# Kernel optimization log

Hardware: AMD Instinct MI355X
Metric: run time of the kernel (lower is better)

## Reference

```python
import jax, jax.numpy as jnp
import numpy as np

EPS = 1e-5

def _mlp(x, w1, b1, w2, b2):
    # torch: Linear -> ReLU -> Linear (weights stored as (in, out))
    return jax.nn.relu(x @ w1 + b1) @ w2 + b2

def _ln(x, g, b):
    mu = x.mean(-1, keepdims=True)
    var = ((x - mu) ** 2).mean(-1, keepdims=True)
    return (x - mu) * jax.lax.rsqrt(var + EPS) * g + b

def setup_inputs():
    key = jax.random.key(0)
    B, N, d, d_out, M, K = 8, 8192, 256, 512, 2048, 16
    ks = jax.random.split(key, 16)
    def nrm(k, shape, s=0.05):
        return jax.random.normal(k, shape, jnp.float32) * s
    return dict(
        pos=jax.random.normal(ks[0], (B, N, 3), jnp.float32),
        feat=jax.random.normal(ks[1], (B, N, d), jnp.float32),
        fps_idx=jax.random.randint(ks[2], (B, M), 0, N, jnp.int32),
        knn_idx=jax.random.randint(ks[3], (B, M, K), 0, N, jnp.int32),
        cs1=16, cs2=64,
        mlp1_w1=nrm(ks[4], (2, 4, d), 0.3), mlp1_b1=jnp.zeros((2, d)),
        mlp1_w2=nrm(ks[5], (2, d, d)), mlp1_b2=jnp.zeros((2, d)),
        mlp2_w1=nrm(ks[6], (2, 6, d), 0.3), mlp2_b1=jnp.zeros((2, d)),
        mlp2_w2=nrm(ks[7], (2, d, d)), mlp2_b2=jnp.zeros((2, d)),
        wq=nrm(ks[8], (2, d, d)), wk=nrm(ks[9], (2, d, d)),
        wv=nrm(ks[10], (2, d, d)), wo=nrm(ks[11], (2, d, d)), bo=jnp.zeros((2, d)),
        ln_g=jnp.ones((2, d)), ln_b=jnp.zeros((2, d)),
        td_w=nrm(ks[12], (d, d_out)), td_b=jnp.zeros((d_out,)),
        bn_g=jnp.ones((d_out,)), bn_b=jnp.zeros((d_out,)),
        bn_mean=jnp.zeros((d_out,)), bn_var=jnp.ones((d_out,)),
    )

def reference(pos, feat, fps_idx, knn_idx, cs1, cs2,
              mlp1_w1, mlp1_b1, mlp1_w2, mlp1_b2,
              mlp2_w1, mlp2_b1, mlp2_w2, mlp2_b2,
              wq, wk, wv, wo, bo, ln_g, ln_b,
              td_w, td_b, bn_g, bn_b, bn_mean, bn_var):
    def block(f_in, cs, i):
        # DLPTBlock with equal-size contiguous clusters of size cs.
        # Note: original forward returns ln1(h_pos + dlsa_out); the ff branch is dead code.
        B, N, d = f_in.shape
        nc = N // cs
        pc = pos.reshape(B, nc, cs, 3)
        fc = f_in.reshape(B, nc, cs, d)
        cog = pc.mean(axis=2, keepdims=True)         # per-cluster center of gravity
        lp = pc - cog                                # local coords
        nrm = jnp.linalg.norm(lp, axis=-1, keepdims=True)
        h_pos = fc + _mlp(jnp.concatenate([lp, nrm], -1),
                          mlp1_w1[i], mlp1_b1[i], mlp1_w2[i], mlp1_b2[i])
        avg = jnp.broadcast_to(lp.mean(axis=2, keepdims=True), lp.shape)
        h_geo = fc + _mlp(jnp.concatenate([avg, lp], -1),
                          mlp2_w1[i], mlp2_b1[i], mlp2_w2[i], mlp2_b2[i])
        q = (h_geo @ wq[i]) / jnp.sqrt(jnp.float32(d))
        k = h_geo @ wk[i]
        v = h_pos @ wv[i]
        a = jax.nn.softmax(jnp.einsum('bcqd,bckd->bcqk', q, k), axis=-1)
        out = jnp.einsum('bcqk,bckd->bcqd', a, v) @ wo[i] + bo[i]
        return _ln(h_pos + out, ln_g[i], ln_b[i]).reshape(B, N, d)

    f = block(feat, cs1, 0)
    f = block(f, cs2, 1)
    # TransitionDown: linear -> BN (eval, running stats) -> relu -> knn max-pool
    f = f @ td_w + td_b
    f = jax.nn.relu((f - bn_mean) * jax.lax.rsqrt(bn_var + EPS) * bn_g + bn_b)
    pos_ds = jnp.take_along_axis(pos, fps_idx[..., None], axis=1)   # (B, M, 3)
    B = f.shape[0]
    f_knn = f[jnp.arange(B)[:, None, None], knn_idx]                # (B, M, K, d_out)
    feat_ds = f_knn.max(axis=2)
    return (pos_ds, feat_ds)
```

## Files before the change

### kernel.cpp

```cpp
#include <hip/hip_runtime.h>
#include <stdint.h>
#include <stddef.h>

typedef __attribute__((ext_vector_type(8))) short bf16x8;
typedef __attribute__((ext_vector_type(4))) float f32x4;
typedef __attribute__((ext_vector_type(8))) unsigned short u16x8;
typedef __attribute__((ext_vector_type(4))) unsigned short u16x4;
typedef __attribute__((ext_vector_type(2))) unsigned short u16x2;

#define DEVINL __device__ __forceinline__

DEVINL unsigned short f2b(float x){
  union { float f; unsigned int u; } v; v.f = x;
  return (unsigned short)((v.u + 0x7FFFu + ((v.u >> 16) & 1u)) >> 16);
}
DEVINL float b2f(unsigned short h){
  union { float f; unsigned int u; } v; v.u = ((unsigned int)h) << 16;
  return v.f;
}

DEVINL void gl_lds16(void* g, void* lds){
  __builtin_amdgcn_global_load_lds(
      (__attribute__((address_space(1))) void*)g,
      (__attribute__((address_space(3))) void*)lds, 16, 0, 0);
}

__global__ __launch_bounds__(256) void prep_k(
    const float* __restrict__ m1w2, const float* __restrict__ m2w2,
    const float* __restrict__ wqp,  const float* __restrict__ wkp,
    const float* __restrict__ wvp,  const float* __restrict__ wop,
    const float* __restrict__ tdw,  const float* __restrict__ tdb,
    const float* __restrict__ bng,  const float* __restrict__ bnb,
    const float* __restrict__ bnm,  const float* __restrict__ bnv,
    unsigned short* __restrict__ wT, float* __restrict__ bns, float* __restrict__ bnt)
{
  int idx = blockIdx.x * 256 + threadIdx.x;
  if (idx < 786432){
    int mat = idx >> 17;
    int e   = idx & 131071;
    int i   = e >> 16;
    int eb  = e & 65535;
    int n = eb >> 8, kx = eb & 255;
    const float* src; float sc = 1.0f;
    if      (mat == 0) src = m1w2;
    else if (mat == 1) src = m2w2;
    else if (mat == 2){ src = wqp; sc = 0.0625f; }
    else if (mat == 3) src = wkp;
    else if (mat == 4) src = wvp;
    else               src = wop;
    wT[idx] = f2b(src[i*65536 + kx*256 + n] * sc);
  } else if (idx < 917504){
    int e = idx - 786432;
    int n = e >> 8, kx = e & 255;
    wT[786432 + e] = f2b(tdw[kx*512 + n]);
  } else if (idx < 918016){
    int c = idx - 917504;
    float s = bng[c] * rsqrtf(bnv[c] + 1e-5f);
    bns[c] = s;
    bnt[c] = (tdb[c] - bnm[c]) * s + bnb[c];
  }
}

__global__ __launch_bounds__(256) void gemm_k(
    const unsigned short* __restrict__ A,
    const unsigned short* __restrict__ Wt,
    unsigned short* __restrict__ out,
    const float* __restrict__ bias,
    const unsigned short* __restrict__ addend,
    const float* __restrict__ bn_s,
    const float* __restrict__ bn_t,
    int ldc)
{
  __shared__ __attribute__((aligned(16))) unsigned short aT[512*8];
  __shared__ __attribute__((aligned(16))) unsigned short bT[512*8];
  __shared__ __attribute__((aligned(16))) unsigned short epi[128*140];

  const int tid  = threadIdx.x;
  const int lane = tid & 63;
  const int wave = tid >> 6;
  const int lrow = lane & 15, lq = lane >> 4;
  const int wr = wave >> 1, wc = wave & 1;
  const int m0 = blockIdx.x * 128;
  const int n0 = blockIdx.y * 128;

  f32x4 acc[4][4] = {};

  int aOff[4], bOff[4];
#pragma unroll
  for (int mt = 0; mt < 4; mt++){
    int row = wr*64 + mt*16 + lrow;
    aOff[mt] = row*64 + ((lq ^ ((row >> 1) & 3)) << 4);
  }
#pragma unroll
  for (int nt = 0; nt < 4; nt++){
    int row = wc*64 + nt*16 + lrow;
    bOff[nt] = row*64 + ((lq ^ ((row >> 1) & 3)) << 4);
  }

  const int s0 = tid, s1 = tid + 256;
  const int r0 = s0 >> 2, kc0 = (s0 & 3) ^ ((r0 >> 1) & 3);
  const int r1 = s1 >> 2, kc1 = (s1 & 3) ^ ((r1 >> 1) & 3);
  const unsigned short* Ab = A  + (size_t)m0 * 256;
  const unsigned short* Bb = Wt + (size_t)n0 * 256;
  char* aL = (char*)aT;
  char* bL = (char*)bT;
  const int wslot = wave * 64 * 16;

  for (int k0 = 0; k0 < 256; k0 += 32){
    __syncthreads();
    gl_lds16((void*)(Ab + r0*256 + k0 + kc0*8), aL + wslot);
    gl_lds16((void*)(Ab + r1*256 + k0 + kc1*8), aL + 4096 + wslot);
    gl_lds16((void*)(Bb + r0*256 + k0 + kc0*8), bL + wslot);
    gl_lds16((void*)(Bb + r1*256 + k0 + kc1*8), bL + 4096 + wslot);
    __syncthreads();
    bf16x8 af[4], bfr[4];
#pragma unroll
    for (int mt = 0; mt < 4; mt++) af[mt]  = *(const bf16x8*)(aL + aOff[mt]);
#pragma unroll
    for (int nt = 0; nt < 4; nt++) bfr[nt] = *(const bf16x8*)(bL + bOff[nt]);
#pragma unroll
    for (int mt = 0; mt < 4; mt++)
#pragma unroll
      for (int nt = 0; nt < 4; nt++)
        acc[mt][nt] = __builtin_amdgcn_mfma_f32_16x16x32_bf16(af[mt], bfr[nt], acc[mt][nt], 0, 0, 0);
  }

  __syncthreads();
#pragma unroll
  for (int mt = 0; mt < 4; mt++){
    int row = wr*64 + mt*16 + lq*4;
#pragma unroll
    for (int nt = 0; nt < 4; nt++){
      int col = wc*64 + nt*16 + lrow;
#pragma unroll
      for (int r = 0; r < 4; r++)
        epi[(row + r)*140 + col] = f2b(acc[mt][nt][r]);
    }
  }
  __syncthreads();

  const int erow = tid >> 1, h = tid & 1;
  const size_t gbase = (size_t)(m0 + erow) * (size_t)ldc + n0;
#pragma unroll
  for (int i = 0; i < 8; i++){
    int col = h*64 + i*8;
    u16x4 lo = *(const u16x4*)(&epi[erow*140 + col]);
    u16x4 hi = *(const u16x4*)(&epi[erow*140 + col + 4]);
    float y[8];
#pragma unroll
    for (int j = 0; j < 4; j++){ y[j] = b2f(lo[j]); y[4+j] = b2f(hi[j]); }
    if (addend){
      u16x8 ad = *(const u16x8*)(addend + gbase + col);
#pragma unroll
      for (int j = 0; j < 8; j++) y[j] += b2f(ad[j]);
    }
    if (bias){
#pragma unroll
      for (int j = 0; j < 8; j++) y[j] += bias[n0 + col + j];
    }
    if (bn_s){
#pragma unroll
      for (int j = 0; j < 8; j++){
        float t2 = y[j]*bn_s[n0 + col + j] + bn_t[n0 + col + j];
        y[j] = fmaxf(t2, 0.f);
      }
    }
    u16x8 o;
#pragma unroll
    for (int j = 0; j < 8; j++) o[j] = f2b(y[j]);
    *(u16x8*)(out + gbase + col) = o;
  }
}

DEVINL void wg_gemm1(const unsigned short* __restrict__ Wt,
                     const char* Als, int tid, f32x4 (&acc)[4])
{
  const int lane = tid & 63;
  const int wave = tid >> 6;
  const int lrow = lane & 15, lq = lane >> 4;
  const unsigned short* base = Wt + (size_t)(wave*16 + lrow)*256 + lq*8;

  bf16x8 bn = *(const bf16x8*)(base);
#pragma unroll
  for (int k = 0; k < 8; k++){
    bf16x8 b = bn;
    if (k < 7) bn = *(const bf16x8*)(base + (k+1)*32);
#pragma unroll
    for (int mt = 0; mt < 4; mt++){
      int row = mt*16 + lrow;
      bf16x8 af = *(const bf16x8*)(Als + row*512 + ((k*64 + lq*16) ^ ((row & 7) << 4)));
      acc[mt] = __builtin_amdgcn_mfma_f32_16x16x32_bf16(af, b, acc[mt], 0, 0, 0);
    }
  }
}

DEVINL void wg_epi_fc1(f32x4 (&acc)[4], char* Yls, const float* __restrict__ bias,
                       const unsigned int (&fcp)[4][2], int tid)
{
  const int lane = tid & 63, wave = tid >> 6;
  const int lrow = lane & 15, lq = lane >> 4;
  const int col = wave*16 + lrow;
  const float bv = bias[col];
#pragma unroll
  for (int mt = 0; mt < 4; mt++){
#pragma unroll
    for (int p = 0; p < 2; p++){
      unsigned int f = fcp[mt][p];
      int row0 = mt*16 + lq*4 + 2*p;
      int row1 = row0 + 1;
      float y0 = acc[mt][2*p]   + bv + b2f((unsigned short)f);
      float y1 = acc[mt][2*p+1] + bv + b2f((unsigned short)(f >> 16));
      *(unsigned short*)(Yls + row0*512 + ((col*2) ^ ((row0 & 7) << 4))) = f2b(y0);
      *(unsigned short*)(Yls + row1*512 + ((col*2) ^ ((row1 & 7) << 4))) = f2b(y1);
    }
  }
}

DEVINL void wg_epi_regs1(f32x4 (&acc)[4], const float* __restrict__ bias,
                         const unsigned int (&fcp)[4][2], unsigned int (&hp)[4][2],
                         int tid)
{
  const int lane = tid & 63, wave = tid >> 6;
  const int lrow = lane & 15;
  const int col = wave*16 + lrow;
  const float bv = bias[col];
#pragma unroll
  for (int mt = 0; mt < 4; mt++){
#pragma unroll
    for (int p = 0; p < 2; p++){
      unsigned int f = fcp[mt][p];
      float y0 = acc[mt][2*p]   + bv + b2f((unsigned short)f);
      float y1 = acc[mt][2*p+1] + bv + b2f((unsigned short)(f >> 16));
      hp[mt][p] = (unsigned int)f2b(y0) | ((unsigned int)f2b(y1) << 16);
    }
  }
}

DEVINL void wg_epi_plain1(f32x4 (&acc)[4], char* Yls, int tid)
{
  const int lane = tid & 63, wave = tid >> 6;
  const int lrow = lane & 15, lq = lane >> 4;
  const int col = wave*16 + lrow;
#pragma unroll
  for (int mt = 0; mt < 4; mt++){
#pragma unroll
    for (int r = 0; r < 4; r++){
      const int row = mt*16 + lq*4 + r;
      *(unsigned short*)(Yls + row*512 + ((col*2) ^ ((row & 7) << 4))) = f2b(acc[mt][r]);
    }
  }
}

DEVINL void wg_epi_vt1(f32x4 (&acc)[4], char* VT, int tid)
{
  const int lane = tid & 63, wave = tid >> 6;
  const int lrow = lane & 15, lq = lane >> 4;
  const int col = wave*16 + lrow;
#pragma unroll
  for (int mt = 0; mt < 4; mt++){
    const int row0 = mt*16 + lq*4;
    u16x4 w;
#pragma unroll
    for (int r = 0; r < 4; r++) w[r] = f2b(acc[mt][r]);
    *(u16x4*)(VT + col*128 + ((row0*2) ^ ((col & 7) << 4))) = w;
  }
}

template<int CS, bool F32IN>
__global__ __launch_bounds__(1024, 4) void block_k(
    const float* __restrict__ pos,
    const float* __restrict__ featF,
    const unsigned short* __restrict__ featB,
    const float* __restrict__ w1a, const float* __restrict__ b1a,
    const float* __restrict__ w1b, const float* __restrict__ b1b,
    const unsigned short* __restrict__ m1w2T, const float* __restrict__ m1b2,
    const unsigned short* __restrict__ m2w2T, const float* __restrict__ m2b2,
    const unsigned short* __restrict__ wqT, const unsigned short* __restrict__ wkT,
    const unsigned short* __restrict__ wvT, const unsigned short* __restrict__ woT,
    const float* __restrict__ bo, const float* __restrict__ lgam,
    const float* __restrict__ lbet,
    unsigned short* __restrict__ out)
{
  __shared__ __attribute__((aligned(16))) char smem[82240];
  char* BA = smem;
  char* BB = smem + 32768;
  char* Pm = smem + 65536;
  float (*P3)[3]    = (float(*)[3])(smem + 73728);
  float (*Cg)[3]    = (float(*)[3])(smem + 74496);
  float (*Gg)[4]    = (float(*)[4])(smem + 74560);
  float (*smx)[4]   = (float(*)[4])(smem + 75584);
  float (*ssm)[4]   = (float(*)[4])(smem + 76608);
  float (*sred)[8]  = (float(*)[8])(smem + 77632);
  float (*s2red)[8] = (float(*)[8])(smem + 79680);
  float* mub = (float*)(smem + 81728);
  float* rsb = (float*)(smem + 81984);

  const int tid  = threadIdx.x;
  const int lane = tid & 63;
  const int wave = tid >> 6;
  const int lrow = lane & 15, lq = lane >> 4;
  const int m0 = blockIdx.x * 64;

  unsigned short* gout = out + (size_t)m0 * 256;

  unsigned int fcp[4][2];
  {
    const int col = wave*16 + lrow;
    if constexpr (F32IN){
      const float* resF = featF + (size_t)m0 * 256;
#pragma unroll
      for (int mt = 0; mt < 4; mt++)
#pragma unroll
        for (int p = 0; p < 2; p++){
          int row0 = mt*16 + lq*4 + 2*p;
          unsigned int lo = f2b(resF[row0*256 + col]);
          unsigned int hi = f2b(resF[(row0+1)*256 + col]);
          fcp[mt][p] = lo | (hi << 16);
        }
    } else {
      const unsigned short* resB = featB + (size_t)m0 * 256;
#pragma unroll
      for (int mt = 0; mt < 4; mt++)
#pragma unroll
        for (int p = 0; p < 2; p++){
          int row0 = mt*16 + lq*4 + 2*p;
          unsigned int lo = resB[row0*256 + col];
          unsigned int hi = resB[(row0+1)*256 + col];
          fcp[mt][p] = lo | (hi << 16);
        }
    }
  }

  if (tid < 64){
    P3[tid][0] = pos[(size_t)(m0+tid)*3 + 0];
    P3[tid][1] = pos[(size_t)(m0+tid)*3 + 1];
    P3[tid][2] = pos[(size_t)(m0+tid)*3 + 2];
  }
  __syncthreads();

  constexpr int NCH = 64 / CS;
  if (tid < NCH*3){
    int ch = tid / 3, c = tid - ch*3;
    float s = 0.f;
    for (int r = 0; r < CS; r++) s += P3[ch*CS + r][c];
    Cg[ch][c] = s / (float)CS;
  }
  __syncthreads();
  if (tid < 64){
    int ch = (CS == 16) ? (tid >> 4) : 0;
    float x = P3[tid][0] - Cg[ch][0];
    float y = P3[tid][1] - Cg[ch][1];
    float z = P3[tid][2] - Cg[ch][2];
    Gg[tid][0] = x; Gg[tid][1] = y; Gg[tid][2] = z;
    Gg[tid][3] = sqrtf(x*x + y*y + z*z);
  }
  __syncthreads();

  {
    const int c = tid & 255;
    const int r0 = (tid >> 8) * 16;
    const float wb0 = w1b[768+c], wb1 = w1b[1024+c], wb2 = w1b[1280+c];
    const float bb  = b1b[c];
    for (int r = r0; r < r0 + 16; r++){
      float v2 = bb + Gg[r][0]*wb0 + Gg[r][1]*wb1 + Gg[r][2]*wb2;
      *(unsigned short*)(BA + r*512 + ((c*2) ^ ((r & 7) << 4))) = f2b(fmaxf(v2, 0.f));
    }
  }
  __syncthreads();
  {
    f32x4 acc[4] = {};
    wg_gemm1(m2w2T, BA, tid, acc);
    wg_epi_fc1(acc, BB, m2b2, fcp, tid);
    __syncthreads();
  }
  {
    const int c = tid & 255;
    const int r0 = (tid >> 8) * 16;
    const float wa0 = w1a[c], wa1 = w1a[256+c], wa2 = w1a[512+c], wa3 = w1a[768+c];
    const float ba  = b1a[c];
    for (int r = r0; r < r0 + 16; r++){
      float v1 = ba + Gg[r][0]*wa0 + Gg[r][1]*wa1 + Gg[r][2]*wa2 + Gg[r][3]*wa3;
      *(unsigned short*)(BA + r*512 + ((c*2) ^ ((r & 7) << 4))) = f2b(fmaxf(v1, 0.f));
    }
  }
  __syncthreads();
  unsigned int hp[4][2];
  {
    f32x4 acc[4] = {};
    wg_gemm1(m1w2T, BA, tid, acc);
    wg_epi_regs1(acc, m1b2, fcp, hp, tid);
    __syncthreads();
  }
  {
    f32x4 acc[4] = {};
    wg_gemm1(wqT, BB, tid, acc);
    wg_epi_plain1(acc, BA, tid);
    __syncthreads();
  }
  {
    f32x4 acc[4] = {};
    wg_gemm1(wkT, BB, tid, acc);
    __syncthreads();
    wg_epi_plain1(acc, BB, tid);
    __syncthreads();
  }

  if (CS == 64){
    const int tr = wave & 3, tc = wave >> 2;
    f32x4 sacc = {};
    const int qrow = tr*16 + lrow;
    const int brow = tc*16 + lrow;
    const int qsw  = (qrow & 7) << 4;
    const int bsw  = (brow & 7) << 4;
#pragma unroll
    for (int kk = 0; kk < 8; kk++){
      bf16x8 aq = *(const bf16x8*)(BA + qrow*512 + ((kk*64 + lq*16) ^ qsw));
      bf16x8 bk = *(const bf16x8*)(BB + brow*512 + ((kk*64 + lq*16) ^ bsw));
      sacc = __builtin_amdgcn_mfma_f32_16x16x32_bf16(aq, bk, sacc, 0, 0, 0);
    }
#pragma unroll
    for (int r = 0; r < 4; r++){
      float m = sacc[r];
#pragma unroll
      for (int d = 1; d < 16; d <<= 1) m = fmaxf(m, __shfl_xor(m, d));
      float e = __expf(sacc[r] - m);
      sacc[r] = e;
      float s = e;
#pragma unroll
      for (int d = 1; d < 16; d <<= 1) s += __shfl_xor(s, d);
      if (lrow == 0){
        int row = tr*16 + lq*4 + r;
        smx[row][tc] = m;
        ssm[row][tc] = s;
      }
    }
    __syncthreads();
#pragma unroll
    for (int r = 0; r < 4; r++){
      int row = tr*16 + lq*4 + r;
      float m0v = smx[row][0], m1v = smx[row][1], m2v = smx[row][2], m3v = smx[row][3];
      float M = fmaxf(fmaxf(m0v, m1v), fmaxf(m2v, m3v));
      float S = ssm[row][0]*__expf(m0v - M) + ssm[row][1]*__expf(m1v - M)
              + ssm[row][2]*__expf(m2v - M) + ssm[row][3]*__expf(m3v - M);
      float f = __expf(smx[row][tc] - M) / S;
      int col = tc*16 + lrow;
      *(unsigned short*)(Pm + row*128 + ((col*2) ^ ((row & 7) << 4))) = f2b(sacc[r]*f);
    }
    __syncthreads();
  } else {
    if (wave < 4){
      f32x4 sacc = {};
      const int qrow = wave*16 + lrow;
      const int qsw  = (qrow & 7) << 4;
#pragma unroll
      for (int kk = 0; kk < 8; kk++){
        bf16x8 aq = *(const bf16x8*)(BA + qrow*512 + ((kk*64 + lq*16) ^ qsw));
        bf16x8 bk = *(const bf16x8*)(BB + qrow*512 + ((kk*64 + lq*16) ^ qsw));
        sacc = __builtin_amdgcn_mfma_f32_16x16x32_bf16(aq, bk, sacc, 0, 0, 0);
      }
#pragma unroll
      for (int r = 0; r < 4; r++){
        float m = sacc[r];
#pragma unroll
        for (int d = 1; d < 16; d <<= 1) m = fmaxf(m, __shfl_xor(m, d));
        float e = __expf(sacc[r] - m);
        float s = e;
#pragma unroll
        for (int d = 1; d < 16; d <<= 1) s += __shfl_xor(s, d);
        int row = wave*16 + lq*4 + r;
        *(unsigned short*)(Pm + row*64 + ((lrow*2) ^ ((row & 3) << 4))) = f2b(e / s);
      }
    } else if (tid < 512){
      int t2 = tid - 256;
      int row = t2 >> 2, j = t2 & 3;
      u16x4 z = {};
      *(u16x4*)(Pm + row*64 + ((32 + j*8) ^ ((row & 3) << 4))) = z;
    }
    __syncthreads();
  }

  {
    const int col = wave*16 + lrow;
#pragma unroll
    for (int mt = 0; mt < 4; mt++)
#pragma unroll
      for (int p = 0; p < 2; p++){
        int row0 = mt*16 + lq*4 + 2*p;
        int row1 = row0 + 1;
        unsigned int d = hp[mt][p];
        *(unsigned short*)(BA + row0*512 + ((col*2) ^ ((row0 & 7) << 4))) = (unsigned short)d;
        *(unsigned short*)(BA + row1*512 + ((col*2) ^ ((row1 & 7) << 4))) = (unsigned short)(d >> 16);
      }
  }
  __syncthreads();
  {
    f32x4 acc[4] = {};
    wg_gemm1(wvT, BA, tid, acc);
    wg_epi_vt1(acc, BB, tid);
    __syncthreads();
  }

  {
    f32x4 oacc[4] = {};
    const int d = wave*16 + lrow;
    const int dsw = (d & 7) << 4;
    if (CS == 64){
#pragma unroll
      for (int kk = 0; kk < 2; kk++){
        bf16x8 bv = *(const bf16x8*)(BB + d*128 + ((kk*64 + lq*16) ^ dsw));
#pragma unroll
        for (int mt = 0; mt < 4; mt++){
          int row = mt*16 + lrow;
          bf16x8 ap = *(const bf16x8*)(Pm + row*128 + ((kk*64 + lq*16) ^ ((row & 7) << 4)));
          oacc[mt] = __builtin_amdgcn_mfma_f32_16x16x32_bf16(ap, bv, oacc[mt], 0, 0, 0);
        }
      }
    } else {
#pragma unroll
      for (int mt = 0; mt < 4; mt++){
        int row = mt*16 + lrow;
        bf16x8 ap = *(const bf16x8*)(Pm + row*64 + ((lq*16) ^ ((row & 3) << 4)));
        bf16x8 bv = *(const bf16x8*)(BB + d*128 + ((mt*32 + (lq & 1)*16) ^ dsw));
        oacc[mt] = __builtin_amdgcn_mfma_f32_16x16x32_bf16(ap, bv, oacc[mt], 0, 0, 0);
      }
    }
#pragma unroll
    for (int mt = 0; mt < 4; mt++){
#pragma unroll
      for (int r = 0; r < 4; r++){
        int row = mt*16 + lq*4 + r;
        *(unsigned short*)(BA + row*512 + ((d*2) ^ ((row & 7) << 4))) = f2b(oacc[mt][r]);
      }
    }
    __syncthreads();
  }

  {
    f32x4 yacc[4] = {};
    wg_gemm1(woT, BA, tid, yacc);
    __syncthreads();
    const int col = wave*16 + lrow;
    const float bov = bo[col];
#pragma unroll
    for (int mt = 0; mt < 4; mt++){
#pragma unroll
      for (int p = 0; p < 2; p++){
        int row0 = mt*16 + lq*4 + 2*p;
        int row1 = row0 + 1;
        unsigned int d = hp[mt][p];
        float z0 = yacc[mt][2*p]   + bov + b2f((unsigned short)d);
        float z1 = yacc[mt][2*p+1] + bov + b2f((unsigned short)(d >> 16));
        *(unsigned short*)(BA + row0*512 + ((col*2) ^ ((row0 & 7) << 4))) = f2b(z0);
        *(unsigned short*)(BA + row1*512 + ((col*2) ^ ((row1 & 7) << 4))) = f2b(z1);
      }
    }
    __syncthreads();
  }
  {
    const int row = (tid >> 3) & 63, part = tid & 7;
    const size_t gr = (size_t)row * 256;
    const int sw = (row & 7) << 4;
    if (tid < 512){
      float sm = 0.f, sq = 0.f;
#pragma unroll
      for (int i = 0; i < 4; i++){
        int col = part*32 + i*8;
        u16x8 v = *(const u16x8*)(BA + row*512 + ((col*2) ^ sw));
#pragma unroll
        for (int j = 0; j < 8; j++){
          float y = b2f(v[j]);
          sm += y; sq += y*y;
        }
      }
      sred[row][part] = sm; s2red[row][part] = sq;
    }
    __syncthreads();
    if (tid < 64){
      float s = 0.f, q2 = 0.f;
#pragma unroll
      for (int p = 0; p < 8; p++){ s += sred[tid][p]; q2 += s2red[tid][p]; }
      float mu = s * (1.0f/256.0f);
      float var = q2 * (1.0f/256.0f) - mu*mu;
      mub[tid] = mu;
      rsb[tid] = rsqrtf(var + 1e-5f);
    }
    __syncthreads();
    if (tid < 512){
      const float mu = mub[row], rs = rsb[row];
#pragma unroll
      for (int i = 0; i < 4; i++){
        int col = part*32 + i*8;
        u16x8 v = *(const u16x8*)(BA + row*512 + ((col*2) ^ sw));
        u16x8 o;
#pragma unroll
        for (int j = 0; j < 8; j++)
          o[j] = f2b((b2f(v[j]) - mu)*rs*lgam[col + j] + lbet[col + j]);
        *(u16x8*)(gout + gr + col) = o;
      }
    }
  }
}

__global__ __launch_bounds__(256) void out_k(
    const unsigned short* __restrict__ F2,
    const float* __restrict__ pos,
    const int* __restrict__ fps,
    const int* __restrict__ knn,
    float* __restrict__ outp)
{
  const int p = blockIdx.x;
  const int b = p >> 11;
  const int t = threadIdx.x;
  const int* kn = knn + (size_t)p * 16;
  const int c = t * 2;
  float m1 = -3.0e38f, m2 = -3.0e38f;
  for (int j = 0; j < 16; j++){
    int idx = kn[j];
    size_t row = ((size_t)b * 8192 + idx) * 512;
    u16x2 v = *(const u16x2*)(F2 + row + c);
    m1 = fmaxf(m1, b2f(v.x));
    m2 = fmaxf(m2, b2f(v.y));
  }
  float* of = outp + 49152 + (size_t)p * 512 + c;
  float2 o; o.x = m1; o.y = m2;
  *(float2*)of = o;
  if (t < 3){
    int fi = fps[p];
    outp[(size_t)p*3 + t] = pos[((size_t)b*8192 + fi)*3 + t];
  }
}

extern "C" void kernel_launch(void* const* d_in, const int* in_sizes, int n_in,
                              void* d_out, int out_size, void* d_ws, size_t ws_size,
                              hipStream_t stream)
{
  (void)in_sizes; (void)n_in; (void)out_size; (void)ws_size;

  const float* pos  = (const float*)d_in[0];
  const float* feat = (const float*)d_in[1];
  const int*   fps  = (const int*)d_in[2];
  const int*   knn  = (const int*)d_in[3];
  const float* m1w1 = (const float*)d_in[6];
  const float* m1b1 = (const float*)d_in[7];
  const float* m1w2 = (const float*)d_in[8];
  const float* m1b2 = (const float*)d_in[9];
  const float* m2w1 = (const float*)d_in[10];
  const float* m2b1 = (const float*)d_in[11];
  const float* m2w2 = (const float*)d_in[12];
  const float* m2b2 = (const float*)d_in[13];
  const float* wq   = (const float*)d_in[14];
  const float* wk   = (const float*)d_in[15];
  const float* wv   = (const float*)d_in[16];
  const float* wo   = (const float*)d_in[17];
  const float* bo   = (const float*)d_in[18];
  const float* lng  = (const float*)d_in[19];
  const float* lnb  = (const float*)d_in[20];
  const float* tdw  = (const float*)d_in[21];
  const float* tdb  = (const float*)d_in[22];
  const float* bng  = (const float*)d_in[23];
  const float* bnb  = (const float*)d_in[24];
  const float* bnm  = (const float*)d_in[25];
  const float* bnv  = (const float*)d_in[26];

  char* ws = (char*)d_ws;
  unsigned short* wT = (unsigned short*)ws;
  float* bns = (float*)(ws + 1835008);
  float* bnt = (float*)(ws + 1837056);
  const size_t SLOT = 33554432;
  unsigned short* A  = (unsigned short*)(ws + 2097152);
  unsigned short* Bs = (unsigned short*)(ws + 2097152 + SLOT);
  unsigned short* E  = (unsigned short*)(ws + 2097152 + 2*SLOT);

  auto wtm = [&](int mat, int i){ return wT + (size_t)mat*131072 + (size_t)i*65536; };
  unsigned short* tdT = wT + 786432;

  prep_k<<<3586, 256, 0, stream>>>(m1w2, m2w2, wq, wk, wv, wo, tdw, tdb, bng, bnb, bnm, bnv,
                                   wT, bns, bnt);

  block_k<16, true><<<1024, 1024, 0, stream>>>(
      pos, feat, nullptr,
      m1w1, m1b1, m2w1, m2b1,
      wtm(0,0), m1b2, wtm(1,0), m2b2,
      wtm(2,0), wtm(3,0), wtm(4,0), wtm(5,0),
      bo, lng, lnb, A);

  block_k<64, false><<<1024, 1024, 0, stream>>>(
      pos, nullptr, A,
      m1w1 + 1024, m1b1 + 256, m2w1 + 1536, m2b1 + 256,
      wtm(0,1), m1b2 + 256, wtm(1,1), m2b2 + 256,
      wtm(2,1), wtm(3,1), wtm(4,1), wtm(5,1),
      bo + 256, lng + 256, lnb + 256, Bs);

  gemm_k<<<dim3(512,4), 256, 0, stream>>>(Bs, tdT, E, nullptr, nullptr, bns, bnt, 512);

  out_k<<<16384, 256, 0, stream>>>(E, pos, fps, knn, (float*)d_out);
}
```

Baseline: 566.5 us.

## Split workgroup into two wave roles running independent GEMMs concurrently

The 16 waves are split into two groups of eight, each computing 64x32 output tiles, so independent GEMM pairs (the two MLP second layers, then Q and K projections) run side by side. This removes several barrier-separated sequential phases. LDS grows from about 82KB to 148KB with four ping-pong buffers, and the residual features are re-read from global memory in the epilogues instead of being held in registers. The extra LDS allows fewer resident workgroups per CU, and the output projection now runs on only half the waves.

```diff
diff --git a/kernel.cpp b/kernel.cpp
--- a/kernel.cpp
+++ b/kernel.cpp
@@ -172,97 +172,139 @@
   }
 }
 
-DEVINL void wg_gemm1(const unsigned short* __restrict__ Wt,
-                     const char* Als, int tid, f32x4 (&acc)[4])
-{
-  const int lane = tid & 63;
-  const int wave = tid >> 6;
+DEVINL void wg_gemm2(const unsigned short* __restrict__ Wt,
+                     const char* Als, int wid8, int lane, f32x4 (&acc)[4][2])
+{
   const int lrow = lane & 15, lq = lane >> 4;
-  const unsigned short* base = Wt + (size_t)(wave*16 + lrow)*256 + lq*8;
-
-  bf16x8 bn = *(const bf16x8*)(base);
+  const unsigned short* base0 = Wt + (size_t)(wid8*32 + lrow)*256 + lq*8;
+  const unsigned short* base1 = base0 + 16*256;
+
+  bf16x8 bn0 = *(const bf16x8*)(base0);
+  bf16x8 bn1 = *(const bf16x8*)(base1);
 #pragma unroll
   for (int k = 0; k < 8; k++){
-    bf16x8 b = bn;
-    if (k < 7) bn = *(const bf16x8*)(base + (k+1)*32);
+    bf16x8 b0 = bn0, b1 = bn1;
+    if (k < 7){
+      bn0 = *(const bf16x8*)(base0 + (k+1)*32);
+      bn1 = *(const bf16x8*)(base1 + (k+1)*32);
+    }
 #pragma unroll
     for (int mt = 0; mt < 4; mt++){
       int row = mt*16 + lrow;
       bf16x8 af = *(const bf16x8*)(Als + row*512 + ((k*64 + lq*16) ^ ((row & 7) << 4)));
-      acc[mt] = __builtin_amdgcn_mfma_f32_16x16x32_bf16(af, b, acc[mt], 0, 0, 0);
-    }
-  }
-}
-
-DEVINL void wg_epi_fc1(f32x4 (&acc)[4], char* Yls, const float* __restrict__ bias,
-                       const unsigned int (&fcp)[4][2], int tid)
-{
-  const int lane = tid & 63, wave = tid >> 6;
+      acc[mt][0] = __builtin_amdgcn_mfma_f32_16x16x32_bf16(af, b0, acc[mt][0], 0, 0, 0);
+      acc[mt][1] = __builtin_amdgcn_mfma_f32_16x16x32_bf16(af, b1, acc[mt][1], 0, 0, 0);
+    }
+  }
+}
+
+template<bool F32RES>
+DEVINL void wg_epi_fcg(f32x4 (&acc)[4][2], char* Yls, const float* __restrict__ bias,
+                       const float* __restrict__ resF,
+                       const unsigned short* __restrict__ resB,
+                       int wid8, int lane)
+{
   const int lrow = lane & 15, lq = lane >> 4;
-  const int col = wave*16 + lrow;
-  const float bv = bias[col];
 #pragma unroll
   for (int mt = 0; mt < 4; mt++){
 #pragma unroll
-    for (int p = 0; p < 2; p++){
-      unsigned int f = fcp[mt][p];
-      int row0 = mt*16 + lq*4 + 2*p;
-      int row1 = row0 + 1;
-      float y0 = acc[mt][2*p]   + bv + b2f((unsigned short)f);
-      float y1 = acc[mt][2*p+1] + bv + b2f((unsigned short)(f >> 16));
-      *(unsigned short*)(Yls + row0*512 + ((col*2) ^ ((row0 & 7) << 4))) = f2b(y0);
-      *(unsigned short*)(Yls + row1*512 + ((col*2) ^ ((row1 & 7) << 4))) = f2b(y1);
-    }
-  }
-}
-
-DEVINL void wg_epi_regs1(f32x4 (&acc)[4], const float* __restrict__ bias,
-                         const unsigned int (&fcp)[4][2], unsigned int (&hp)[4][2],
-                         int tid)
-{
-  const int lane = tid & 63, wave = tid >> 6;
-  const int lrow = lane & 15;
-  const int col = wave*16 + lrow;
-  const float bv = bias[col];
+    for (int nt = 0; nt < 2; nt++){
+      const int col = wid8*32 + nt*16 + lrow;
+      const float bv = bias[col];
+#pragma unroll
+      for (int r = 0; r < 4; r++){
+        const int row = mt*16 + lq*4 + r;
+        float fc = F32RES ? resF[row*256 + col] : b2f(resB[row*256 + col]);
+        float y = acc[mt][nt][r] + bv + fc;
+        *(unsigned short*)(Yls + row*512 + ((col*2) ^ ((row & 7) << 4))) = f2b(y);
+      }
+    }
+  }
+}
+
+template<bool F32RES>
+DEVINL void wg_epi_regs_fcg(f32x4 (&acc)[4][2], const float* __restrict__ bias,
+                            const float* __restrict__ resF,
+                            const unsigned short* __restrict__ resB,
+                            unsigned int (&hp)[4][2][2], int wid8, int lane)
+{
+  const int lrow = lane & 15, lq = lane >> 4;
 #pragma unroll
   for (int mt = 0; mt < 4; mt++){
 #pragma unroll
-    for (int p = 0; p < 2; p++){
-      unsigned int f = fcp[mt][p];
-      float y0 = acc[mt][2*p]   + bv + b2f((unsigned short)f);
-      float y1 = acc[mt][2*p+1] + bv + b2f((unsigned short)(f >> 16));
-      hp[mt][p] = (unsigned int)f2b(y0) | ((unsigned int)f2b(y1) << 16);
-    }
-  }
-}
-
-DEVINL void wg_epi_plain1(f32x4 (&acc)[4], char* Yls, int tid)
-{
-  const int lane = tid & 63, wave = tid >> 6;
+    for (int nt = 0; nt < 2; nt++){
+      const int col = wid8*32 + nt*16 + lrow;
+      const float bv = bias[col];
+#pragma unroll
+      for (int p = 0; p < 2; p++){
+        int row0 = mt*16 + lq*4 + 2*p;
+        float fc0 = F32RES ? resF[row0*256 + col] : b2f(resB[row0*256 + col]);
+        float fc1 = F32RES ? resF[(row0+1)*256 + col] : b2f(resB[(row0+1)*256 + col]);
+        float y0 = acc[mt][nt][2*p]   + bv + fc0;
+        float y1 = acc[mt][nt][2*p+1] + bv + fc1;
+        hp[mt][nt][p] = (unsigned int)f2b(y0) | ((unsigned int)f2b(y1) << 16);
+      }
+    }
+  }
+}
+
+DEVINL void wg_epi_plain2(f32x4 (&acc)[4][2], char* Yls, int wid8, int lane)
+{
   const int lrow = lane & 15, lq = lane >> 4;
-  const int col = wave*16 + lrow;
 #pragma unroll
   for (int mt = 0; mt < 4; mt++){
 #pragma unroll
-    for (int r = 0; r < 4; r++){
-      const int row = mt*16 + lq*4 + r;
-      *(unsigned short*)(Yls + row*512 + ((col*2) ^ ((row & 7) << 4))) = f2b(acc[mt][r]);
-    }
-  }
-}
-
-DEVINL void wg_epi_vt1(f32x4 (&acc)[4], char* VT, int tid)
-{
-  const int lane = tid & 63, wave = tid >> 6;
+    for (int nt = 0; nt < 2; nt++){
+      const int col = wid8*32 + nt*16 + lrow;
+#pragma unroll
+      for (int r = 0; r < 4; r++){
+        const int row = mt*16 + lq*4 + r;
+        *(unsigned short*)(Yls + row*512 + ((col*2) ^ ((row & 7) << 4))) = f2b(acc[mt][nt][r]);
+      }
+    }
+  }
+}
+
+DEVINL void wg_gemm_v(const unsigned short* __restrict__ Wt,
+                      const char* Als, int wm, int wn, int lane, f32x4 (&acc)[2][2])
+{
   const int lrow = lane & 15, lq = lane >> 4;
-  const int col = wave*16 + lrow;
-#pragma unroll
-  for (int mt = 0; mt < 4; mt++){
-    const int row0 = mt*16 + lq*4;
-    u16x4 w;
-#pragma unroll
-    for (int r = 0; r < 4; r++) w[r] = f2b(acc[mt][r]);
-    *(u16x4*)(VT + col*128 + ((row0*2) ^ ((col & 7) << 4))) = w;
+  const unsigned short* base0 = Wt + (size_t)(wn*32 + lrow)*256 + lq*8;
+  const unsigned short* base1 = base0 + 16*256;
+
+  bf16x8 bn0 = *(const bf16x8*)(base0);
+  bf16x8 bn1 = *(const bf16x8*)(base1);
+#pragma unroll
+  for (int k = 0; k < 8; k++){
+    bf16x8 b0 = bn0, b1 = bn1;
+    if (k < 7){
+      bn0 = *(const bf16x8*)(base0 + (k+1)*32);
+      bn1 = *(const bf16x8*)(base1 + (k+1)*32);
+    }
+#pragma unroll
+    for (int mt = 0; mt < 2; mt++){
+      int row = wm*32 + mt*16 + lrow;
+      bf16x8 af = *(const bf16x8*)(Als + row*512 + ((k*64 + lq*16) ^ ((row & 7) << 4)));
+      acc[mt][0] = __builtin_amdgcn_mfma_f32_16x16x32_bf16(af, b0, acc[mt][0], 0, 0, 0);
+      acc[mt][1] = __builtin_amdgcn_mfma_f32_16x16x32_bf16(af, b1, acc[mt][1], 0, 0, 0);
+    }
+  }
+}
+
+DEVINL void wg_epi_vt2(f32x4 (&acc)[2][2], char* VT, int wm, int wn, int lane)
+{
+  const int lrow = lane & 15, lq = lane >> 4;
+#pragma unroll
+  for (int mt = 0; mt < 2; mt++){
+#pragma unroll
+    for (int nt = 0; nt < 2; nt++){
+      const int col  = wn*32 + nt*16 + lrow;
+      const int row0 = wm*32 + mt*16 + lq*4;
+      u16x4 w;
+#pragma unroll
+      for (int r = 0; r < 4; r++) w[r] = f2b(acc[mt][nt][r]);
+      *(u16x4*)(VT + col*128 + ((row0*2) ^ ((col & 7) << 4))) = w;
+    }
   }
 }
 
@@ -281,55 +323,35 @@
     const float* __restrict__ lbet,
     unsigned short* __restrict__ out)
 {
-  __shared__ __attribute__((aligned(16))) char smem[82240];
-  char* BA = smem;
-  char* BB = smem + 32768;
-  char* Pm = smem + 65536;
-  float (*P3)[3]    = (float(*)[3])(smem + 73728);
-  float (*Cg)[3]    = (float(*)[3])(smem + 74496);
-  float (*Gg)[4]    = (float(*)[4])(smem + 74560);
-  float (*smx)[4]   = (float(*)[4])(smem + 75584);
-  float (*ssm)[4]   = (float(*)[4])(smem + 76608);
-  float (*sred)[8]  = (float(*)[8])(smem + 77632);
-  float (*s2red)[8] = (float(*)[8])(smem + 79680);
-  float* mub = (float*)(smem + 81728);
-  float* rsb = (float*)(smem + 81984);
+  __shared__ __attribute__((aligned(16))) char smem[147776];
+  char* B0 = smem;
+  char* B1 = smem + 32768;
+  char* B2 = smem + 65536;
+  char* B3 = smem + 98304;
+  char* Pm = smem + 131072;
+  float (*P3)[3]    = (float(*)[3])(smem + 139264);
+  float (*Cg)[3]    = (float(*)[3])(smem + 140032);
+  float (*Gg)[4]    = (float(*)[4])(smem + 140096);
+  float (*smx)[4]   = (float(*)[4])(smem + 141120);
+  float (*ssm)[4]   = (float(*)[4])(smem + 142144);
+  float (*sred)[8]  = (float(*)[8])(smem + 143168);
+  float (*s2red)[8] = (float(*)[8])(smem + 145216);
+  float* mub = (float*)(smem + 147264);
+  float* rsb = (float*)(smem + 147520);
 
   const int tid  = threadIdx.x;
   const int lane = tid & 63;
   const int wave = tid >> 6;
+  const int wid8 = wave & 7;
+  const int role = wave >> 3;
   const int lrow = lane & 15, lq = lane >> 4;
   const int m0 = blockIdx.x * 64;
 
   unsigned short* gout = out + (size_t)m0 * 256;
-
-  unsigned int fcp[4][2];
-  {
-    const int col = wave*16 + lrow;
-    if constexpr (F32IN){
-      const float* resF = featF + (size_t)m0 * 256;
-#pragma unroll
-      for (int mt = 0; mt < 4; mt++)
-#pragma unroll
-        for (int p = 0; p < 2; p++){
-          int row0 = mt*16 + lq*4 + 2*p;
-          unsigned int lo = f2b(resF[row0*256 + col]);
-          unsigned int hi = f2b(resF[(row0+1)*256 + col]);
-          fcp[mt][p] = lo | (hi << 16);
-        }
-    } else {
-      const unsigned short* resB = featB + (size_t)m0 * 256;
-#pragma unroll
-      for (int mt = 0; mt < 4; mt++)
-#pragma unroll
-        for (int p = 0; p < 2; p++){
-          int row0 = mt*16 + lq*4 + 2*p;
-          unsigned int lo = resB[row0*256 + col];
-          unsigned int hi = resB[(row0+1)*256 + col];
-          fcp[mt][p] = lo | (hi << 16);
-        }
-    }
-  }
+  const float* resF = nullptr;
+  const unsigned short* resB = nullptr;
+  if constexpr (F32IN) resF = featF + (size_t)m0 * 256;
+  else                 resB = featB + (size_t)m0 * 256;
 
   if (tid < 64){
     P3[tid][0] = pos[(size_t)(m0+tid)*3 + 0];
@@ -357,53 +379,68 @@
   __syncthreads();
 
   {
-    const int c = tid & 255;
-    const int r0 = (tid >> 8) * 16;
-    const float wb0 = w1b[768+c], wb1 = w1b[1024+c], wb2 = w1b[1280+c];
-    const float bb  = b1b[c];
-    for (int r = r0; r < r0 + 16; r++){
-      float v2 = bb + Gg[r][0]*wb0 + Gg[r][1]*wb1 + Gg[r][2]*wb2;
-      *(unsigned short*)(BA + r*512 + ((c*2) ^ ((r & 7) << 4))) = f2b(fmaxf(v2, 0.f));
-    }
-  }
-  __syncthreads();
+    if (tid < 512){
+      const int c = tid & 255;
+      const int r0 = (tid >> 8) * 32;
+      const float wb0 = w1b[768+c], wb1 = w1b[1024+c], wb2 = w1b[1280+c];
+      const float bb  = b1b[c];
+      for (int r = r0; r < r0 + 32; r++){
+        float v2 = bb + Gg[r][0]*wb0 + Gg[r][1]*wb1 + Gg[r][2]*wb2;
+        *(unsigned short*)(B0 + r*512 + ((c*2) ^ ((r & 7) << 4))) = f2b(fmaxf(v2, 0.f));
+      }
+    } else {
+      const int t = tid - 512;
+      const int c = t & 255;
+      const int r0 = (t >> 8) * 32;
+      const float wa0 = w1a[c], wa1 = w1a[256+c], wa2 = w1a[512+c], wa3 = w1a[768+c];
+      const float ba  = b1a[c];
+      for (int r = r0; r < r0 + 32; r++){
+        float v1 = ba + Gg[r][0]*wa0 + Gg[r][1]*wa1 + Gg[r][2]*wa2 + Gg[r][3]*wa3;
+        *(unsigned short*)(B1 + r*512 + ((c*2) ^ ((r & 7) << 4))) = f2b(fmaxf(v1, 0.f));
+      }
+    }
+  }
+  __syncthreads();
+
+  unsigned int hp[4][2][2];
   {
-    f32x4 acc[4] = {};
-    wg_gemm1(m2w2T, BA, tid, acc);
-    wg_epi_fc1(acc, BB, m2b2, fcp, tid);
-    __syncthreads();
-  }
+    if (role == 0){
+      f32x4 acc[4][2] = {};
+      wg_gemm2(m2w2T, B0, wid8, lane, acc);
+      wg_epi_fcg<F32IN>(acc, B2, m2b2, resF, resB, wid8, lane);
+    } else {
+      f32x4 acc[4][2] = {};
+      wg_gemm2(m1w2T, B1, wid8, lane, acc);
+      wg_epi_regs_fcg<F32IN>(acc, m1b2, resF, resB, hp, wid8, lane);
+    }
+  }
+  __syncthreads();
+
   {
-    const int c = tid & 255;
-    const int r0 = (tid >> 8) * 16;
-    const float wa0 = w1a[c], wa1 = w1a[256+c], wa2 = w1a[512+c], wa3 = w1a[768+c];
-    const float ba  = b1a[c];
-    for (int r = r0; r < r0 + 16; r++){
-      float v1 = ba + Gg[r][0]*wa0 + Gg[r][1]*wa1 + Gg[r][2]*wa2 + Gg[r][3]*wa3;
-      *(unsigned short*)(BA + r*512 + ((c*2) ^ ((r & 7) << 4))) = f2b(fmaxf(v1, 0.f));
-    }
-  }
-  __syncthreads();
-  unsigned int hp[4][2];
-  {
-    f32x4 acc[4] = {};
-    wg_gemm1(m1w2T, BA, tid, acc);
-    wg_epi_regs1(acc, m1b2, fcp, hp, tid);
-    __syncthreads();
-  }
-  {
-    f32x4 acc[4] = {};
-    wg_gemm1(wqT, BB, tid, acc);
-    wg_epi_plain1(acc, BA, tid);
-    __syncthreads();
-  }
-  {
-    f32x4 acc[4] = {};
-    wg_gemm1(wkT, BB, tid, acc);
-    __syncthreads();
-    wg_epi_plain1(acc, BB, tid);
-    __syncthreads();
-  }
+    if (role == 0){
+      f32x4 acc[4][2] = {};
+      wg_gemm2(wqT, B2, wid8, lane, acc);
+      wg_epi_plain2(acc, B1, wid8, lane);
+    } else {
+#pragma unroll
+      for (int mt = 0; mt < 4; mt++)
+#pragma unroll
+        for (int nt = 0; nt < 2; nt++)
+#pragma unroll
+          for (int p = 0; p < 2; p++){
+            int col = wid8*32 + nt*16 + lrow;
+            int row0 = mt*16 + lq*4 + 2*p;
+            int row1 = row0 + 1;
+            unsigned int d = hp[mt][nt][p];
+            *(unsigned short*)(B0 + row0*512 + ((col*2) ^ ((row0 & 7) << 4))) = (unsigned short)d;
+            *(unsigned short*)(B0 + row1*512 + ((col*2) ^ ((row1 & 7) << 4))) = (unsigned short)(d >> 16);
+          }
+      f32x4 acc[4][2] = {};
+      wg_gemm2(wkT, B2, wid8, lane, acc);
+      wg_epi_plain2(acc, B3, wid8, lane);
+    }
+  }
+  __syncthreads();
 
   if (CS == 64){
     const int tr = wave & 3, tc = wave >> 2;
@@ -414,8 +451,8 @@
     const int bsw  = (brow & 7) << 4;
 #pragma unroll
     for (int kk = 0; kk < 8; kk++){
-      bf16x8 aq = *(const bf16x8*)(BA + qrow*512 + ((kk*64 + lq*16) ^ qsw));
-      bf16x8 bk = *(const bf16x8*)(BB + brow*512 + ((kk*64 + lq*16) ^ bsw));
+      bf16x8 aq = *(const bf16x8*)(B1 + qrow*512 + ((kk*64 + lq*16) ^ qsw));
+      bf16x8 bk = *(const bf16x8*)(B3 + brow*512 + ((kk*64 + lq*16) ^ bsw));
       sacc = __builtin_amdgcn_mfma_f32_16x16x32_bf16(aq, bk, sacc, 0, 0, 0);
     }
 #pragma unroll
@@ -454,8 +491,8 @@
       const int qsw  = (qrow & 7) << 4;
 #pragma unroll
       for (int kk = 0; kk < 8; kk++){
-        bf16x8 aq = *(const bf16x8*)(BA + qrow*512 + ((kk*64 + lq*16) ^ qsw));
-        bf16x8 bk = *(const bf16x8*)(BB + qrow*512 + ((kk*64 + lq*16) ^ qsw));
+        bf16x8 aq = *(const bf16x8*)(B1 + qrow*512 + ((kk*64 + lq*16) ^ qsw));
+        bf16x8 bk = *(const bf16x8*)(B3 + qrow*512 + ((kk*64 + lq*16) ^ qsw));
         sacc = __builtin_amdgcn_mfma_f32_16x16x32_bf16(aq, bk, sacc, 0, 0, 0);
       }
 #pragma unroll
@@ -480,25 +517,12 @@
   }
 
   {
-    const int col = wave*16 + lrow;
-#pragma unroll
-    for (int mt = 0; mt < 4; mt++)
-#pragma unroll
-      for (int p = 0; p < 2; p++){
-        int row0 = mt*16 + lq*4 + 2*p;
-        int row1 = row0 + 1;
-        unsigned int d = hp[mt][p];
-        *(unsigned short*)(BA + row0*512 + ((col*2) ^ ((row0 & 7) << 4))) = (unsigned short)d;
-        *(unsigned short*)(BA + row1*512 + ((col*2) ^ ((row1 & 7) << 4))) = (unsigned short)(d >> 16);
-      }
-  }
-  __syncthreads();
-  {
-    f32x4 acc[4] = {};
-    wg_gemm1(wvT, BA, tid, acc);
-    wg_epi_vt1(acc, BB, tid);
-    __syncthreads();
-  }
+    const int wm = wave >> 3, wn = wave & 7;
+    f32x4 acc[2][2] = {};
+    wg_gemm_v(wvT, B0, wm, wn, lane, acc);
+    wg_epi_vt2(acc, B2, wm, wn, lane);
+  }
+  __syncthreads();
 
   {
     f32x4 oacc[4] = {};
@@ -507,7 +531,7 @@
     if (CS == 64){
 #pragma unroll
       for (int kk = 0; kk < 2; kk++){
-        bf16x8 bv = *(const bf16x8*)(BB + d*128 + ((kk*64 + lq*16) ^ dsw));
+        bf16x8 bv = *(const bf16x8*)(B2 + d*128 + ((kk*64 + lq*16) ^ dsw));
 #pragma unroll
         for (int mt = 0; mt < 4; mt++){
           int row = mt*16 + lrow;
@@ -520,7 +544,7 @@
       for (int mt = 0; mt < 4; mt++){
         int row = mt*16 + lrow;
         bf16x8 ap = *(const bf16x8*)(Pm + row*64 + ((lq*16) ^ ((row & 3) << 4)));
-        bf16x8 bv = *(const bf16x8*)(BB + d*128 + ((mt*32 + (lq & 1)*16) ^ dsw));
+        bf16x8 bv = *(const bf16x8*)(B2 + d*128 + ((mt*32 + (lq & 1)*16) ^ dsw));
         oacc[mt] = __builtin_amdgcn_mfma_f32_16x16x32_bf16(ap, bv, oacc[mt], 0, 0, 0);
       }
     }
@@ -529,33 +553,38 @@
 #pragma unroll
       for (int r = 0; r < 4; r++){
         int row = mt*16 + lq*4 + r;
-        *(unsigned short*)(BA + row*512 + ((d*2) ^ ((row & 7) << 4))) = f2b(oacc[mt][r]);
-      }
-    }
-    __syncthreads();
-  }
+        *(unsigned short*)(B3 + row*512 + ((d*2) ^ ((row & 7) << 4))) = f2b(oacc[mt][r]);
+      }
+    }
+  }
+  __syncthreads();
 
   {
-    f32x4 yacc[4] = {};
-    wg_gemm1(woT, BA, tid, yacc);
-    __syncthreads();
-    const int col = wave*16 + lrow;
-    const float bov = bo[col];
-#pragma unroll
-    for (int mt = 0; mt < 4; mt++){
-#pragma unroll
-      for (int p = 0; p < 2; p++){
-        int row0 = mt*16 + lq*4 + 2*p;
-        int row1 = row0 + 1;
-        unsigned int d = hp[mt][p];
-        float z0 = yacc[mt][2*p]   + bov + b2f((unsigned short)d);
-        float z1 = yacc[mt][2*p+1] + bov + b2f((unsigned short)(d >> 16));
-        *(unsigned short*)(BA + row0*512 + ((col*2) ^ ((row0 & 7) << 4))) = f2b(z0);
-        *(unsigned short*)(BA + row1*512 + ((col*2) ^ ((row1 & 7) << 4))) = f2b(z1);
-      }
-    }
-    __syncthreads();
-  }
+    if (role == 1){
+      f32x4 yacc[4][2] = {};
+      wg_gemm2(woT, B3, wid8, lane, yacc);
+#pragma unroll
+      for (int mt = 0; mt < 4; mt++){
+#pragma unroll
+        for (int nt = 0; nt < 2; nt++){
+          const int col = wid8*32 + nt*16 + lrow;
+          const float bov = bo[col];
+#pragma unroll
+          for (int p = 0; p < 2; p++){
+            unsigned int d = hp[mt][nt][p];
+            int row0 = mt*16 + lq*4 + 2*p;
+            int row1 = row0 + 1;
+            float z0 = yacc[mt][nt][2*p]   + bov + b2f((unsigned short)d);
+            float z1 = yacc[mt][nt][2*p+1] + bov + b2f((unsigned short)(d >> 16));
+            *(unsigned short*)(B1 + row0*512 + ((col*2) ^ ((row0 & 7) << 4))) = f2b(z0);
+            *(unsigned short*)(B1 + row1*512 + ((col*2) ^ ((row1 & 7) << 4))) = f2b(z1);
+          }
+        }
+      }
+    }
+  }
+  __syncthreads();
+
   {
     const int row = (tid >> 3) & 63, part = tid & 7;
     const size_t gr = (size_t)row * 256;
@@ -565,7 +594,7 @@
 #pragma unroll
       for (int i = 0; i < 4; i++){
         int col = part*32 + i*8;
-        u16x8 v = *(const u16x8*)(BA + row*512 + ((col*2) ^ sw));
+        u16x8 v = *(const u16x8*)(B1 + row*512 + ((col*2) ^ sw));
 #pragma unroll
         for (int j = 0; j < 8; j++){
           float y = b2f(v[j]);
@@ -590,7 +619,7 @@
 #pragma unroll
       for (int i = 0; i < 4; i++){
         int col = part*32 + i*8;
-        u16x8 v = *(const u16x8*)(BA + row*512 + ((col*2) ^ sw));
+        u16x8 v = *(const u16x8*)(B1 + row*512 + ((col*2) ^ sw));
         u16x8 o;
 #pragma unroll
         for (int j = 0; j < 8; j++)
```

Measured after the change: 611.8 us. 1.08x slower.

## Load full K-extent tiles into LDS once and use 512-thread GEMM blocks

Applied to the files above, without the earlier changes.

The transition-down GEMM now issues all global-to-LDS loads for the whole K=256 extent of both A and W tiles up front, using one barrier instead of two per 32-wide K step. The block grows to 8 waves, each computing a 32x64 sub-tile, and the epilogue is split across four threads per row. This removes per-iteration barrier stalls and exposes more memory parallelism. In exchange it needs 128KB of LDS per block, which limits occupancy to about one block per CU, so the launch_bounds hint of 2 blocks may not hold.

```diff
diff --git a/kernel.cpp b/kernel.cpp
--- a/kernel.cpp
+++ b/kernel.cpp
@@ -61,7 +61,7 @@
   }
 }
 
-__global__ __launch_bounds__(256) void gemm_k(
+__global__ __launch_bounds__(512, 2) void gemm_k(
     const unsigned short* __restrict__ A,
     const unsigned short* __restrict__ Wt,
     unsigned short* __restrict__ out,
@@ -71,24 +71,38 @@
     const float* __restrict__ bn_t,
     int ldc)
 {
-  __shared__ __attribute__((aligned(16))) unsigned short aT[512*8];
-  __shared__ __attribute__((aligned(16))) unsigned short bT[512*8];
-  __shared__ __attribute__((aligned(16))) unsigned short epi[128*140];
+  __shared__ __attribute__((aligned(16))) char smem[131072];
+  char* aL = smem;
+  char* bL = smem + 65536;
+  unsigned short* epi = (unsigned short*)smem;
 
   const int tid  = threadIdx.x;
   const int lane = tid & 63;
   const int wave = tid >> 6;
   const int lrow = lane & 15, lq = lane >> 4;
-  const int wr = wave >> 1, wc = wave & 1;
+  const int wr = wave & 3, wc = wave >> 2;
   const int m0 = blockIdx.x * 128;
   const int n0 = blockIdx.y * 128;
 
-  f32x4 acc[4][4] = {};
-
-  int aOff[4], bOff[4];
-#pragma unroll
-  for (int mt = 0; mt < 4; mt++){
-    int row = wr*64 + mt*16 + lrow;
+  {
+    const int r  = tid >> 2;
+    const int kc = (tid & 3) ^ ((r >> 1) & 3);
+    const unsigned short* Ab = A  + (size_t)(m0 + r) * 256 + kc*8;
+    const unsigned short* Bb = Wt + (size_t)(n0 + r) * 256 + kc*8;
+    const int wslot = wave * 1024;
+#pragma unroll
+    for (int k0 = 0; k0 < 8; k0++){
+      gl_lds16((void*)(Ab + k0*32), aL + k0*8192 + wslot);
+      gl_lds16((void*)(Bb + k0*32), bL + k0*8192 + wslot);
+    }
+  }
+  __syncthreads();
+
+  f32x4 acc[2][4] = {};
+  int aOff[2], bOff[4];
+#pragma unroll
+  for (int mt = 0; mt < 2; mt++){
+    int row = wr*32 + mt*16 + lrow;
     aOff[mt] = row*64 + ((lq ^ ((row >> 1) & 3)) << 4);
   }
 #pragma unroll
@@ -96,30 +110,15 @@
     int row = wc*64 + nt*16 + lrow;
     bOff[nt] = row*64 + ((lq ^ ((row >> 1) & 3)) << 4);
   }
-
-  const int s0 = tid, s1 = tid + 256;
-  const int r0 = s0 >> 2, kc0 = (s0 & 3) ^ ((r0 >> 1) & 3);
-  const int r1 = s1 >> 2, kc1 = (s1 & 3) ^ ((r1 >> 1) & 3);
-  const unsigned short* Ab = A  + (size_t)m0 * 256;
-  const unsigned short* Bb = Wt + (size_t)n0 * 256;
-  char* aL = (char*)aT;
-  char* bL = (char*)bT;
-  const int wslot = wave * 64 * 16;
-
-  for (int k0 = 0; k0 < 256; k0 += 32){
-    __syncthreads();
-    gl_lds16((void*)(Ab + r0*256 + k0 + kc0*8), aL + wslot);
-    gl_lds16((void*)(Ab + r1*256 + k0 + kc1*8), aL + 4096 + wslot);
-    gl_lds16((void*)(Bb + r0*256 + k0 + kc0*8), bL + wslot);
-    gl_lds16((void*)(Bb + r1*256 + k0 + kc1*8), bL + 4096 + wslot);
-    __syncthreads();
-    bf16x8 af[4], bfr[4];
-#pragma unroll
-    for (int mt = 0; mt < 4; mt++) af[mt]  = *(const bf16x8*)(aL + aOff[mt]);
-#pragma unroll
-    for (int nt = 0; nt < 4; nt++) bfr[nt] = *(const bf16x8*)(bL + bOff[nt]);
-#pragma unroll
-    for (int mt = 0; mt < 4; mt++)
+#pragma unroll
+  for (int k0 = 0; k0 < 8; k0++){
+    bf16x8 af[2], bfr[4];
+#pragma unroll
+    for (int mt = 0; mt < 2; mt++) af[mt]  = *(const bf16x8*)(aL + k0*8192 + aOff[mt]);
+#pragma unroll
+    for (int nt = 0; nt < 4; nt++) bfr[nt] = *(const bf16x8*)(bL + k0*8192 + bOff[nt]);
+#pragma unroll
+    for (int mt = 0; mt < 2; mt++)
 #pragma unroll
       for (int nt = 0; nt < 4; nt++)
         acc[mt][nt] = __builtin_amdgcn_mfma_f32_16x16x32_bf16(af[mt], bfr[nt], acc[mt][nt], 0, 0, 0);
@@ -127,8 +126,8 @@
 
   __syncthreads();
 #pragma unroll
-  for (int mt = 0; mt < 4; mt++){
-    int row = wr*64 + mt*16 + lq*4;
+  for (int mt = 0; mt < 2; mt++){
+    int row = wr*32 + mt*16 + lq*4;
 #pragma unroll
     for (int nt = 0; nt < 4; nt++){
       int col = wc*64 + nt*16 + lrow;
@@ -139,11 +138,11 @@
   }
   __syncthreads();
 
-  const int erow = tid >> 1, h = tid & 1;
+  const int erow = tid >> 2, h = tid & 3;
   const size_t gbase = (size_t)(m0 + erow) * (size_t)ldc + n0;
 #pragma unroll
-  for (int i = 0; i < 8; i++){
-    int col = h*64 + i*8;
+  for (int i = 0; i < 4; i++){
+    int col = h*32 + i*8;
     u16x4 lo = *(const u16x4*)(&epi[erow*140 + col]);
     u16x4 hi = *(const u16x4*)(&epi[erow*140 + col + 4]);
     float y[8];
@@ -691,7 +690,7 @@
       wtm(2,1), wtm(3,1), wtm(4,1), wtm(5,1),
       bo + 256, lng + 256, lnb + 256, Bs);
 
-  gemm_k<<<dim3(512,4), 256, 0, stream>>>(Bs, tdT, E, nullptr, nullptr, bns, bnt, 512);
+  gemm_k<<<dim3(512,4), 512, 0, stream>>>(Bs, tdT, E, nullptr, nullptr, bns, bnt, 512);
 
   out_k<<<16384, 256, 0, stream>>>(E, pos, fps, knn, (float*)d_out);
 }
```

Result: slower. 586.7 us (+3.6%).
